# Kernel optimization log

Measured on AMD Instinct MI355X. Metric: run time of the kernel, lower is better.

The kernel has to match this reference:

```python
import jax, jax.numpy as jnp
import numpy as np
from jax import lax


def setup_inputs() -> dict:
    key = jax.random.key(0)
    k1, k2 = jax.random.split(key)
    B, C, H, W = 8, 16, 128, 128
    rate = 2
    hs = H // rate
    hw = hs * hs
    x = jax.random.normal(k1, (B, C, H, W), dtype=jnp.float32)
    scores = jax.random.normal(k2, (B, hw, hw), dtype=jnp.float32)
    alpha = jnp.ones((1,), dtype=jnp.float32)
    return {"x": x, "scores": scores, "alpha": alpha}


def reference(x, scores, alpha):
    B, C, H, W = x.shape
    P = scores.shape[2]              # hw = hs*ws
    hs = int(np.sqrt(P))
    ws = hs
    rate = H // hs
    vk = 2 * rate                    # vksize
    pad = rate // 2                  # vpadding (ReplicationPad2d)

    # --- extract_patches: replication pad + unfold(kernel=vk, stride=rate) ---
    xp = jnp.pad(x, ((0, 0), (0, 0), (pad, pad), (pad, pad)), mode='edge')
    ii = (jnp.arange(hs) * rate)[:, None] + jnp.arange(vk)[None, :]   # [hs, vk]
    jj = (jnp.arange(ws) * rate)[:, None] + jnp.arange(vk)[None, :]   # [ws, vk]
    # gather overlapping patches: [B, C, hs, vk, ws, vk]
    V = xp[:, :, ii][:, :, :, :, jj]
    # -> [B, hs*ws, C, vk, vk] matching torch layout (B, hs, ws, C, vk, vk)
    V = V.transpose(0, 2, 4, 1, 3, 5).reshape(B, hs * ws, C, vk, vk)

    # --- scores: permute(0,2,1) then reshape to per-patch spatial maps ---
    S = scores.transpose(0, 2, 1).reshape(B, P, hs, ws)  # channel p = key index

    # --- grouped conv_transpose2d(stride=rate, padding=pad, groups=B) ---
    # torch conv_transpose2d == lhs-dilated conv with flipped, transposed kernel
    # and padding (vk - 1 - pad) per side; vmapped over batch (one group each).
    w_pad = vk - 1 - pad

    def conv_t(s, v):
        # s: [P, hs, ws] (input channels = patches); v: [P, C, vk, vk]
        w = jnp.flip(v, axis=(-2, -1)).transpose(1, 0, 2, 3)  # [C, P, vk, vk]
        out = lax.conv_general_dilated(
            s[None], w,
            window_strides=(1, 1),
            padding=[(w_pad, w_pad), (w_pad, w_pad)],
            lhs_dilation=(rate, rate),
            dimension_numbers=('NCHW', 'OIHW', 'NCHW'))
        return out[0]  # [C, H, W]

    y = jax.vmap(conv_t)(S, V) / 4.0  # [B, C, H, W]
    return x + y * alpha
```

## Files before the change

kernel.cpp:

```cpp
#include <hip/hip_runtime.h>
#include <hip/hip_bf16.h>

typedef float f32x4 __attribute__((ext_vector_type(4)));
typedef short bf16x8 __attribute__((ext_vector_type(8)));
typedef unsigned short us8 __attribute__((ext_vector_type(8)));
typedef unsigned short us4 __attribute__((ext_vector_type(4)));

__device__ __forceinline__ unsigned short f2bf(float f) {
  union { float f; unsigned u; } v; v.f = f;
  return (unsigned short)((v.u + 0x8000u) >> 16);
}
__device__ __forceinline__ float bf2f(unsigned short u) {
  union { unsigned u; float f; } v; v.u = ((unsigned)u) << 16;
  return v.f;
}

__global__ __launch_bounds__(256) void prep_vmat(const float* __restrict__ x,
                                                 unsigned short* __restrict__ vmatT) {
  int t = blockIdx.x * 256 + threadIdx.x;
  int pc = t & 511;
  int n  = (t >> 9) & 255;
  int b  = t >> 17;
  int c = n >> 4, u = (n >> 2) & 3, v = n & 3;
  int pi = pc >> 3;
  int pj0 = (pc & 7) << 3;
  int row = 2 * pi + u - 1;
  row = row < 0 ? 0 : (row > 127 ? 127 : row);
  const float* xr = x + ((size_t)(b * 16 + c) * 128 + row) * 128;
  us8 o;
#pragma unroll
  for (int e = 0; e < 8; ++e) {
    int col = 2 * (pj0 + e) + v - 1;
    col = col < 0 ? 0 : (col > 127 ? 127 : col);
    o[e] = f2bf(xr[col]);
  }
  *reinterpret_cast<us8*>(vmatT + (size_t)t * 8) = o;
}

__global__ __launch_bounds__(512, 2) void gemm_scores_vmat(
    const float* __restrict__ scores,
    const unsigned short* __restrict__ vmatT,
    unsigned short* __restrict__ Amat) {
  __shared__ unsigned short ldsB[2][32768];

  int bid = blockIdx.x;
  int batch = bid & 7;
  int qb = (bid >> 3) << 7;
  const int phase = (bid >> 3) & 31;

  const int t = threadIdx.x;
  const int lane = t & 63;
  const int wq = t >> 6;
  const int l15 = lane & 15, l16 = lane >> 4;

  const float* aLane =
      scores + ((size_t)(batch * 4096 + qb + wq * 16 + l15)) * 4096 + l16 * 8;
  const unsigned short* Vb = vmatT + (size_t)batch * 256 * 4096;

  const unsigned short* bSrc[8];
#pragma unroll
  for (int i = 0; i < 8; ++i) {
    int c = t + i * 512;
    int gs = (c & 15) ^ ((c >> 4) & 15);
    bSrc[i] = Vb + (size_t)(c >> 4) * 4096 + gs * 8;
  }

  f32x4 acc[16];
#pragma unroll
  for (int ni = 0; ni < 16; ++ni) acc[ni] = (f32x4){0.f, 0.f, 0.f, 0.f};

  f32x4 rE[8], rO[8];
  bf16x8 fa[4];

#define SB __builtin_amdgcn_sched_barrier(0)
#define STAGE_B(kt, bufi)                                                     \
  {                                                                           \
    int kp_ = ((kt) + phase) & 31;                                            \
    _Pragma("unroll") for (int i = 0; i < 8; ++i)                             \
        __builtin_amdgcn_global_load_lds(                                     \
            (const __attribute__((address_space(1))) void*)(bSrc[i] + (size_t)kp_ * 128), \
            (__attribute__((address_space(3))) void*)&ldsB[bufi][(t + i * 512) * 8], \
            16, 0, 0);                                                        \
  }
#define LOAD_A(kt, rr)                                                        \
  {                                                                           \
    int kp_ = ((kt) + phase) & 31;                                            \
    const float* ap_ = aLane + (size_t)kp_ * 128;                             \
    rr[0] = *(const f32x4*)(ap_);                                             \
    rr[1] = *(const f32x4*)(ap_ + 4);                                         \
    rr[2] = *(const f32x4*)(ap_ + 32);                                        \
    rr[3] = *(const f32x4*)(ap_ + 36);                                        \
    rr[4] = *(const f32x4*)(ap_ + 64);                                        \
    rr[5] = *(const f32x4*)(ap_ + 68);                                        \
    rr[6] = *(const f32x4*)(ap_ + 96);                                        \
    rr[7] = *(const f32x4*)(ap_ + 100);                                       \
  }
#define CONV(rr)                                                              \
  {                                                                           \
    _Pragma("unroll") for (int f = 0; f < 4; ++f)                             \
        _Pragma("unroll") for (int e = 0; e < 4; ++e) {                       \
      fa[f][e]     = (short)f2bf(rr[2 * f][e]);                               \
      fa[f][e + 4] = (short)f2bf(rr[2 * f + 1][e]);                           \
    }                                                                         \
  }
#define MFMAS(bufi)                                                           \
  {                                                                           \
    _Pragma("unroll") for (int ks = 0; ks < 4; ++ks)                          \
        _Pragma("unroll") for (int ni = 0; ni < 16; ++ni) {                   \
      int pos = ((ks * 4 + l16) ^ l15) << 3;                                  \
      bf16x8 bv = *(const bf16x8*)(&ldsB[bufi][0] +                           \
                                   (ni * 16 + l15) * 128 + pos);              \
      acc[ni] = __builtin_amdgcn_mfma_f32_16x16x32_bf16(fa[ks], bv, acc[ni],  \
                                                        0, 0, 0);             \
    }                                                                         \
  }
#define BODY(b_, kt, rr)                                                      \
  {                                                                           \
    CONV(rr);                                      \
    SB;                                                                       \
    STAGE_B((kt) + 1, (b_) ^ 1);                                              \
    SB;                                                                       \
    LOAD_A((kt) + 2, rr);                                                     \
    SB;                                                                       \
    MFMAS(b_);                                                                \
    SB;                                                                       \
    asm volatile("s_waitcnt vmcnt(8)" ::: "memory");                          \
    SB;                                                                       \
    __builtin_amdgcn_s_barrier();                                             \
    SB;                                                                       \
  }

  STAGE_B(0, 0);
  SB;
  LOAD_A(0, rE);
  SB;
  LOAD_A(1, rO);
  SB;
  asm volatile("s_waitcnt vmcnt(8)" ::: "memory");
  SB;
  __builtin_amdgcn_s_barrier();
  SB;

  for (int kt = 0; kt < 32; kt += 2) {
    BODY(0, kt, rE);
    BODY(1, kt + 1, rO);
  }

  asm volatile("" ::"v"(rE[0][0]), "v"(rE[3][0]), "v"(rE[5][0]), "v"(rE[7][0]),
               "v"(rO[0][0]), "v"(rO[3][0]), "v"(rO[5][0]), "v"(rO[7][0]));

#undef SB
#undef STAGE_B
#undef LOAD_A
#undef CONV
#undef MFMAS
#undef BODY

  unsigned short* Ao = Amat + ((size_t)(batch * 4096 + qb + wq * 16)) * 256;
#pragma unroll
  for (int ni = 0; ni < 16; ++ni)
#pragma unroll
    for (int j = 0; j < 4; ++j)
      Ao[(size_t)(l16 * 4 + j) * 256 + ni * 16 + l15] = f2bf(acc[ni][j]);
}

__global__ __launch_bounds__(256) void epilogue_kernel(
    const float* __restrict__ x, const unsigned short* __restrict__ Amat,
    const float* __restrict__ alpha, float* __restrict__ out) {
  __shared__ unsigned short L[2 * 64 * 66];

  int b = blockIdx.x >> 7;
  int h = blockIdx.x & 127;
  int t = threadIdx.x;

  int ihi = (h + 1) >> 1, u_hi = (h + 1) & 1;
  bool p0ok = (ihi <= 63), p1ok = (ihi >= 1);
  const unsigned short* Ab = Amat + (size_t)b * 4096 * 256;

  unsigned int* Lw = reinterpret_cast<unsigned int*>(L);
#pragma unroll
  for (int p = 0; p < 2; ++p) {
    bool ok = p ? p1ok : p0ok;
    int rbase = (p ? (ihi - 1) : ihi) * 64;
    int u = u_hi + 2 * p;
#pragma unroll
    for (int i = 0; i < 4; ++i) {
      int q = t + 256 * i;
      int j = q >> 4, c = q & 15;
      us4 ch = (us4){0, 0, 0, 0};
      if (ok)
        ch = *reinterpret_cast<const us4*>(Ab + (size_t)(rbase + j) * 256 +
                                           c * 16 + u * 4);
      int widx = (p * 4224 + j * 66 + c * 4) >> 1;
      Lw[widx]     = (unsigned int)(unsigned short)ch[0] |
                     ((unsigned int)(unsigned short)ch[1] << 16);
      Lw[widx + 1] = (unsigned int)(unsigned short)ch[2] |
                     ((unsigned int)(unsigned short)ch[3] << 16);
    }
  }
  __syncthreads();

  int w = t & 127;
  int cg = t >> 7;
  int jhi = (w + 1) >> 1, v_hi = (w + 1) & 1;
  bool vj_hi = (jhi <= 63), vj_lo = (jhi >= 1);
  float al = alpha[0] * 0.25f;

#pragma unroll
  for (int cc = 0; cc < 8; ++cc) {
    int c = cg * 8 + cc;
    float s = 0.f;
    if (vj_hi) {
      int o = jhi * 66 + c * 4 + v_hi;
      s += bf2f(L[o]) + bf2f(L[4224 + o]);
    }
    if (vj_lo) {
      int o = (jhi - 1) * 66 + c * 4 + v_hi + 2;
      s += bf2f(L[o]) + bf2f(L[4224 + o]);
    }
    size_t xi = (((size_t)b * 16 + c) * 128 + h) * 128 + w;
    out[xi] = x[xi] + al * s;
  }
}

extern "C" void kernel_launch(void* const* d_in, const int* in_sizes, int n_in,
                              void* d_out, int out_size, void* d_ws, size_t ws_size,
                              hipStream_t stream) {
  const float* x      = (const float*)d_in[0];
  const float* scores = (const float*)d_in[1];
  const float* alpha  = (const float*)d_in[2];
  float* out = (float*)d_out;

  unsigned short* vmatT = (unsigned short*)d_ws;
  unsigned short* Amat  = (unsigned short*)((char*)d_ws + (size_t)16 * 1024 * 1024);

  prep_vmat<<<4096, 256, 0, stream>>>(x, vmatT);
  gemm_scores_vmat<<<256, 512, 0, stream>>>(scores, vmatT, Amat);
  epilogue_kernel<<<1024, 256, 0, stream>>>(x, Amat, alpha, out);
}
```

Measured before the change: 164.3 us.

## Switch GEMM to 32x32x16 MFMA with split-K across two wave groups

```diff
diff --git a/kernel.cpp b/kernel.cpp
--- a/kernel.cpp
+++ b/kernel.cpp
@@ -2,6 +2,7 @@
 #include <hip/hip_bf16.h>
 
 typedef float f32x4 __attribute__((ext_vector_type(4)));
+typedef float f32x16 __attribute__((ext_vector_type(16)));
 typedef short bf16x8 __attribute__((ext_vector_type(8)));
 typedef unsigned short us8 __attribute__((ext_vector_type(8)));
 typedef unsigned short us4 __attribute__((ext_vector_type(4)));
@@ -41,7 +42,7 @@
     const float* __restrict__ scores,
     const unsigned short* __restrict__ vmatT,
     unsigned short* __restrict__ Amat) {
-  __shared__ unsigned short ldsB[2][32768];
+  __shared__ unsigned short ldsB[2][2][16384];
 
   int bid = blockIdx.x;
   int batch = bid & 7;
@@ -51,23 +52,30 @@
   const int t = threadIdx.x;
   const int lane = t & 63;
   const int wq = t >> 6;
-  const int l15 = lane & 15, l16 = lane >> 4;
-
-  const float* aLane =
-      scores + ((size_t)(batch * 4096 + qb + wq * 16 + l15)) * 4096 + l16 * 8;
-  const unsigned short* Vb = vmatT + (size_t)batch * 256 * 4096;
-
+  const int g = wq >> 2;
+  const int wv = wq & 3;
+  const int l31 = lane & 31, lhi = lane >> 5;
+
+  const size_t kbase = (size_t)g * 2048;
+  const float* aLane = scores +
+      ((size_t)(batch * 4096 + qb + wv * 32 + l31)) * 4096 + kbase + lhi * 8;
+
+  const int st = t & 255, st_g = t >> 8;
+  const unsigned short* Vb =
+      vmatT + (size_t)batch * 256 * 4096 + (size_t)st_g * 2048;
   const unsigned short* bSrc[8];
 #pragma unroll
   for (int i = 0; i < 8; ++i) {
-    int c = t + i * 512;
-    int gs = (c & 15) ^ ((c >> 4) & 15);
-    bSrc[i] = Vb + (size_t)(c >> 4) * 4096 + gs * 8;
-  }
-
-  f32x4 acc[16];
-#pragma unroll
-  for (int ni = 0; ni < 16; ++ni) acc[ni] = (f32x4){0.f, 0.f, 0.f, 0.f};
+    int c = st + i * 256;
+    int gs = (c & 7) ^ ((c >> 3) & 7);
+    bSrc[i] = Vb + (size_t)(c >> 3) * 4096 + gs * 8;
+  }
+
+  f32x16 acc[8];
+#pragma unroll
+  for (int nb = 0; nb < 8; ++nb)
+#pragma unroll
+    for (int e = 0; e < 16; ++e) acc[nb][e] = 0.f;
 
   f32x4 rE[8], rO[8];
   bf16x8 fa[4];
@@ -78,39 +86,39 @@
     int kp_ = ((kt) + phase) & 31;                                            \
     _Pragma("unroll") for (int i = 0; i < 8; ++i)                             \
         __builtin_amdgcn_global_load_lds(                                     \
-            (const __attribute__((address_space(1))) void*)(bSrc[i] + (size_t)kp_ * 128), \
-            (__attribute__((address_space(3))) void*)&ldsB[bufi][(t + i * 512) * 8], \
+            (const __attribute__((address_space(1))) void*)(bSrc[i] + (size_t)kp_ * 64), \
+            (__attribute__((address_space(3))) void*)&ldsB[st_g][bufi][(st + i * 256) * 8], \
             16, 0, 0);                                                        \
   }
 #define LOAD_A(kt, rr)                                                        \
   {                                                                           \
     int kp_ = ((kt) + phase) & 31;                                            \
-    const float* ap_ = aLane + (size_t)kp_ * 128;                             \
+    const float* ap_ = aLane + (size_t)kp_ * 64;                              \
     rr[0] = *(const f32x4*)(ap_);                                             \
     rr[1] = *(const f32x4*)(ap_ + 4);                                         \
-    rr[2] = *(const f32x4*)(ap_ + 32);                                        \
-    rr[3] = *(const f32x4*)(ap_ + 36);                                        \
-    rr[4] = *(const f32x4*)(ap_ + 64);                                        \
-    rr[5] = *(const f32x4*)(ap_ + 68);                                        \
-    rr[6] = *(const f32x4*)(ap_ + 96);                                        \
-    rr[7] = *(const f32x4*)(ap_ + 100);                                       \
+    rr[2] = *(const f32x4*)(ap_ + 16);                                        \
+    rr[3] = *(const f32x4*)(ap_ + 20);                                        \
+    rr[4] = *(const f32x4*)(ap_ + 32);                                        \
+    rr[5] = *(const f32x4*)(ap_ + 36);                                        \
+    rr[6] = *(const f32x4*)(ap_ + 48);                                        \
+    rr[7] = *(const f32x4*)(ap_ + 52);                                        \
   }
 #define CONV(rr)                                                              \
   {                                                                           \
-    _Pragma("unroll") for (int f = 0; f < 4; ++f)                             \
+    _Pragma("unroll") for (int kb = 0; kb < 4; ++kb)                          \
         _Pragma("unroll") for (int e = 0; e < 4; ++e) {                       \
-      fa[f][e]     = (short)f2bf(rr[2 * f][e]);                               \
-      fa[f][e + 4] = (short)f2bf(rr[2 * f + 1][e]);                           \
+      fa[kb][e]     = (short)f2bf(rr[2 * kb][e]);                             \
+      fa[kb][e + 4] = (short)f2bf(rr[2 * kb + 1][e]);                         \
     }                                                                         \
   }
 #define MFMAS(bufi)                                                           \
   {                                                                           \
-    _Pragma("unroll") for (int ks = 0; ks < 4; ++ks)                          \
-        _Pragma("unroll") for (int ni = 0; ni < 16; ++ni) {                   \
-      int pos = ((ks * 4 + l16) ^ l15) << 3;                                  \
-      bf16x8 bv = *(const bf16x8*)(&ldsB[bufi][0] +                           \
-                                   (ni * 16 + l15) * 128 + pos);              \
-      acc[ni] = __builtin_amdgcn_mfma_f32_16x16x32_bf16(fa[ks], bv, acc[ni],  \
+    _Pragma("unroll") for (int kb = 0; kb < 4; ++kb)                          \
+        _Pragma("unroll") for (int nb = 0; nb < 8; ++nb) {                    \
+      int row_ = nb * 32 + l31;                                               \
+      int pos_ = (kb * 2 + lhi) ^ (l31 & 7);                                  \
+      bf16x8 bv = *(const bf16x8*)(&ldsB[g][bufi][0] + row_ * 64 + pos_ * 8); \
+      acc[nb] = __builtin_amdgcn_mfma_f32_32x32x16_bf16(fa[kb], bv, acc[nb],  \
                                                         0, 0, 0);             \
     }                                                                         \
   }
@@ -156,12 +164,28 @@
 #undef MFMAS
 #undef BODY
 
-  unsigned short* Ao = Amat + ((size_t)(batch * 4096 + qb + wq * 16)) * 256;
-#pragma unroll
-  for (int ni = 0; ni < 16; ++ni)
-#pragma unroll
-    for (int j = 0; j < 4; ++j)
-      Ao[(size_t)(l16 * 4 + j) * 256 + ni * 16 + l15] = f2bf(acc[ni][j]);
+  __syncthreads();
+  float* ldsF = reinterpret_cast<float*>(&ldsB[0][0][0]);
+  if (g == 1) {
+#pragma unroll
+    for (int nb = 0; nb < 8; ++nb)
+#pragma unroll
+      for (int r = 0; r < 16; ++r)
+        ldsF[((wv * 128) + nb * 16 + r) * 64 + lane] = acc[nb][r];
+  }
+  __syncthreads();
+  if (g == 0) {
+    unsigned short* Ao =
+        Amat + ((size_t)(batch * 4096 + qb + wv * 32)) * 256;
+#pragma unroll
+    for (int nb = 0; nb < 8; ++nb)
+#pragma unroll
+      for (int r = 0; r < 16; ++r) {
+        float s = acc[nb][r] + ldsF[((wv * 128) + nb * 16 + r) * 64 + lane];
+        int row = (r & 3) + 8 * (r >> 2) + 4 * lhi;
+        Ao[(size_t)row * 256 + nb * 32 + l31] = f2bf(s);
+      }
+  }
 }
 
 __global__ __launch_bounds__(256) void epilogue_kernel(
```

Result: slower. 215.7 us (+31.3%).

## Retile scores×V GEMM into 2x4 warp grid with 4-stage LDS pipeline

Applied to the files above, without the earlier changes.

```diff
diff --git a/kernel.cpp b/kernel.cpp
--- a/kernel.cpp
+++ b/kernel.cpp
@@ -41,127 +41,154 @@
     const float* __restrict__ scores,
     const unsigned short* __restrict__ vmatT,
     unsigned short* __restrict__ Amat) {
-  __shared__ unsigned short ldsB[2][32768];
+  __shared__ unsigned short lds[4][12288];
 
   int bid = blockIdx.x;
   int batch = bid & 7;
-  int qb = (bid >> 3) << 7;
-  const int phase = (bid >> 3) & 31;
+  int qbi = bid >> 3;
+  int qb = qbi << 7;
+  const int phase = (qbi * 4) & 127;
 
   const int t = threadIdx.x;
   const int lane = t & 63;
   const int wq = t >> 6;
+  const int wm = wq >> 2, wn = wq & 3;
   const int l15 = lane & 15, l16 = lane >> 4;
 
-  const float* aLane =
-      scores + ((size_t)(batch * 4096 + qb + wq * 16 + l15)) * 4096 + l16 * 8;
+  const float* aSrc0 =
+      scores + ((size_t)(batch * 4096 + qb + (t >> 3))) * 4096 + (t & 7) * 4;
+  const float* aSrc1 = aSrc0 + (size_t)64 * 4096;
+  const int aW = (t >> 3) * 32 + ((((t & 7) >> 1) ^ ((t >> 4) & 3)) << 3) +
+                 (t & 1) * 4;
+
   const unsigned short* Vb = vmatT + (size_t)batch * 256 * 4096;
-
-  const unsigned short* bSrc[8];
-#pragma unroll
-  for (int i = 0; i < 8; ++i) {
+  const unsigned short* bSrc[2];
+  int bDst[2];
+#pragma unroll
+  for (int i = 0; i < 2; ++i) {
     int c = t + i * 512;
-    int gs = (c & 15) ^ ((c >> 4) & 15);
-    bSrc[i] = Vb + (size_t)(c >> 4) * 4096 + gs * 8;
-  }
-
-  f32x4 acc[16];
-#pragma unroll
-  for (int ni = 0; ni < 16; ++ni) acc[ni] = (f32x4){0.f, 0.f, 0.f, 0.f};
-
-  f32x4 rE[8], rO[8];
-  bf16x8 fa[4];
+    int gs = (c & 3) ^ ((c >> 3) & 3);
+    bSrc[i] = Vb + (size_t)(c >> 2) * 4096 + gs * 8;
+    bDst[i] = 4096 + c * 8;
+  }
+
+  const int rsw = (l16 ^ ((l15 >> 1) & 3)) << 3;
+  const int aR = (wm * 64 + l15) * 32 + rsw;
+  const int bR = 4096 + (wn * 64 + l15) * 32 + rsw;
+
+  f32x4 acc[4][4];
+#pragma unroll
+  for (int mi = 0; mi < 4; ++mi)
+#pragma unroll
+    for (int ni = 0; ni < 4; ++ni) acc[mi][ni] = (f32x4){0.f, 0.f, 0.f, 0.f};
+
+  f32x4 a0[2], a1[2], a2[2], a3[2];
 
 #define SB __builtin_amdgcn_sched_barrier(0)
-#define STAGE_B(kt, bufi)                                                     \
-  {                                                                           \
-    int kp_ = ((kt) + phase) & 31;                                            \
-    _Pragma("unroll") for (int i = 0; i < 8; ++i)                             \
+#define STAGE_B(kt, sl)                                                       \
+  {                                                                           \
+    int kp_ = ((kt) + phase) & 127;                                           \
+    _Pragma("unroll") for (int i = 0; i < 2; ++i)                             \
         __builtin_amdgcn_global_load_lds(                                     \
-            (const __attribute__((address_space(1))) void*)(bSrc[i] + (size_t)kp_ * 128), \
-            (__attribute__((address_space(3))) void*)&ldsB[bufi][(t + i * 512) * 8], \
+            (const __attribute__((address_space(1))) void*)(bSrc[i] + (size_t)kp_ * 32), \
+            (__attribute__((address_space(3))) void*)&lds[sl][bDst[i]],       \
             16, 0, 0);                                                        \
   }
-#define LOAD_A(kt, rr)                                                        \
-  {                                                                           \
-    int kp_ = ((kt) + phase) & 31;                                            \
-    const float* ap_ = aLane + (size_t)kp_ * 128;                             \
-    rr[0] = *(const f32x4*)(ap_);                                             \
-    rr[1] = *(const f32x4*)(ap_ + 4);                                         \
-    rr[2] = *(const f32x4*)(ap_ + 32);                                        \
-    rr[3] = *(const f32x4*)(ap_ + 36);                                        \
-    rr[4] = *(const f32x4*)(ap_ + 64);                                        \
-    rr[5] = *(const f32x4*)(ap_ + 68);                                        \
-    rr[6] = *(const f32x4*)(ap_ + 96);                                        \
-    rr[7] = *(const f32x4*)(ap_ + 100);                                       \
-  }
-#define CONV(rr)                                                              \
-  {                                                                           \
-    _Pragma("unroll") for (int f = 0; f < 4; ++f)                             \
-        _Pragma("unroll") for (int e = 0; e < 4; ++e) {                       \
-      fa[f][e]     = (short)f2bf(rr[2 * f][e]);                               \
-      fa[f][e + 4] = (short)f2bf(rr[2 * f + 1][e]);                           \
+#define LOAD_AF(kt, rr)                                                       \
+  {                                                                           \
+    int kp_ = ((kt) + phase) & 127;                                           \
+    rr[0] = *(const f32x4*)(aSrc0 + (size_t)kp_ * 32);                        \
+    rr[1] = *(const f32x4*)(aSrc1 + (size_t)kp_ * 32);                        \
+  }
+#define CONVW(rr, sl)                                                         \
+  {                                                                           \
+    us4 p0, p1;                                                               \
+    _Pragma("unroll") for (int e = 0; e < 4; ++e) {                           \
+      p0[e] = f2bf(rr[0][e]);                                                 \
+      p1[e] = f2bf(rr[1][e]);                                                 \
     }                                                                         \
-  }
-#define MFMAS(bufi)                                                           \
-  {                                                                           \
-    _Pragma("unroll") for (int ks = 0; ks < 4; ++ks)                          \
-        _Pragma("unroll") for (int ni = 0; ni < 16; ++ni) {                   \
-      int pos = ((ks * 4 + l16) ^ l15) << 3;                                  \
-      bf16x8 bv = *(const bf16x8*)(&ldsB[bufi][0] +                           \
-                                   (ni * 16 + l15) * 128 + pos);              \
-      acc[ni] = __builtin_amdgcn_mfma_f32_16x16x32_bf16(fa[ks], bv, acc[ni],  \
-                                                        0, 0, 0);             \
-    }                                                                         \
-  }
-#define BODY(b_, kt, rr)                                                      \
-  {                                                                           \
-    CONV(rr);                                      \
-    SB;                                                                       \
-    STAGE_B((kt) + 1, (b_) ^ 1);                                              \
-    SB;                                                                       \
-    LOAD_A((kt) + 2, rr);                                                     \
-    SB;                                                                       \
-    MFMAS(b_);                                                                \
-    SB;                                                                       \
+    *(us4*)&lds[sl][aW] = p0;                                                 \
+    *(us4*)&lds[sl][aW + 2048] = p1;                                          \
+  }
+#define MFMAS(sl)                                                             \
+  {                                                                           \
+    bf16x8 af[4], bv[4];                                                      \
+    _Pragma("unroll") for (int mi = 0; mi < 4; ++mi)                          \
+        af[mi] = *(const bf16x8*)(&lds[sl][0] + aR + mi * 512);               \
+    _Pragma("unroll") for (int ni = 0; ni < 4; ++ni)                          \
+        bv[ni] = *(const bf16x8*)(&lds[sl][0] + bR + ni * 512);               \
+    _Pragma("unroll") for (int mi = 0; mi < 4; ++mi)                          \
+        _Pragma("unroll") for (int ni = 0; ni < 4; ++ni)                      \
+            acc[mi][ni] = __builtin_amdgcn_mfma_f32_16x16x32_bf16(            \
+                af[mi], bv[ni], acc[mi][ni], 0, 0, 0);                        \
+  }
+#define BODY(kt, sC, sS, sW, cs, ls)                                          \
+  {                                                                           \
+    CONVW(cs, sW);                                                            \
+    SB;                                                                       \
+    STAGE_B((kt) + 3, sS);                                                    \
+    SB;                                                                       \
+    LOAD_AF((kt) + 4, ls);                                                    \
+    SB;                                                                       \
+    MFMAS(sC);                                                                \
+    SB;                                                                       \
+    asm volatile("s_waitcnt lgkmcnt(0)" ::: "memory");                        \
     asm volatile("s_waitcnt vmcnt(8)" ::: "memory");                          \
     SB;                                                                       \
     __builtin_amdgcn_s_barrier();                                             \
     SB;                                                                       \
   }
 
+  LOAD_AF(0, a0);
+  SB;
+  LOAD_AF(1, a1);
+  SB;
   STAGE_B(0, 0);
   SB;
-  LOAD_A(0, rE);
-  SB;
-  LOAD_A(1, rO);
-  SB;
-  asm volatile("s_waitcnt vmcnt(8)" ::: "memory");
+  asm volatile("s_waitcnt vmcnt(0)" ::: "memory");
+  SB;
+  CONVW(a0, 0);
+  SB;
+  STAGE_B(1, 1);
+  SB;
+  LOAD_AF(2, a2);
+  SB;
+  STAGE_B(2, 2);
+  SB;
+  LOAD_AF(3, a3);
+  SB;
+  asm volatile("s_waitcnt lgkmcnt(0)" ::: "memory");
   SB;
   __builtin_amdgcn_s_barrier();
   SB;
 
-  for (int kt = 0; kt < 32; kt += 2) {
-    BODY(0, kt, rE);
-    BODY(1, kt + 1, rO);
-  }
-
-  asm volatile("" ::"v"(rE[0][0]), "v"(rE[3][0]), "v"(rE[5][0]), "v"(rE[7][0]),
-               "v"(rO[0][0]), "v"(rO[3][0]), "v"(rO[5][0]), "v"(rO[7][0]));
+  for (int kt = 0; kt < 128; kt += 4) {
+    BODY(kt + 0, 0, 3, 1, a1, a0);
+    BODY(kt + 1, 1, 0, 2, a2, a1);
+    BODY(kt + 2, 2, 1, 3, a3, a2);
+    BODY(kt + 3, 3, 2, 0, a0, a3);
+  }
+
+  asm volatile("" ::"v"(a0[0][0]), "v"(a0[1][0]), "v"(a1[0][0]), "v"(a1[1][0]),
+               "v"(a2[0][0]), "v"(a2[1][0]), "v"(a3[0][0]), "v"(a3[1][0]));
 
 #undef SB
 #undef STAGE_B
-#undef LOAD_A
-#undef CONV
+#undef LOAD_AF
+#undef CONVW
 #undef MFMAS
 #undef BODY
 
-  unsigned short* Ao = Amat + ((size_t)(batch * 4096 + qb + wq * 16)) * 256;
-#pragma unroll
-  for (int ni = 0; ni < 16; ++ni)
-#pragma unroll
-    for (int j = 0; j < 4; ++j)
-      Ao[(size_t)(l16 * 4 + j) * 256 + ni * 16 + l15] = f2bf(acc[ni][j]);
+  unsigned short* Ao =
+      Amat + ((size_t)(batch * 4096 + qb + wm * 64)) * 256 + wn * 64;
+#pragma unroll
+  for (int mi = 0; mi < 4; ++mi)
+#pragma unroll
+    for (int ni = 0; ni < 4; ++ni)
+#pragma unroll
+      for (int j = 0; j < 4; ++j)
+        Ao[(size_t)(mi * 16 + l16 * 4 + j) * 256 + ni * 16 + l15] =
+            f2bf(acc[mi][ni][j]);
 }
 
 __global__ __launch_bounds__(256) void epilogue_kernel(
```

Measured after the change: 169.1 us. 2.9% more time.
